# Kernel tuning notes

Hardware: AMD Instinct MI355X
Metric: run time of the kernel (lower is better)

## Reference

```python
import jax, jax.numpy as jnp
import numpy as np

EMBED, VOCAB, NUM_DIGEST, EXPAND = 128, 50257, 4, 4


def _mueller_hash(k):
    # https://stackoverflow.com/a/12996028 , uint32 wraparound semantics
    k = (k >> np.uint32(16) ^ k) * np.uint32(73244475)
    k = (k >> np.uint32(16) ^ k) * np.uint32(73244475)
    k = k >> np.uint32(16) ^ k
    return k


def setup_inputs() -> dict:
    key = jax.random.key(0)
    k_tok, k_tab, k_w1, k_w2 = jax.random.split(key, 4)
    # bloom ledger hash indices (exact replication of bloom_ledger)
    ids = np.arange(VOCAB, dtype=np.uint32)
    i_list, j_list = [], []
    for _ in range(NUM_DIGEST):
        ids = _mueller_hash(ids)
        i_list.append(ids % VOCAB)
        ids = _mueller_hash(ids)
        j_list.append(ids % VOCAB)
    bloom_i = jnp.asarray(np.concatenate(i_list).astype(np.int32))
    bloom_j = jnp.asarray(np.concatenate(j_list).astype(np.int32))
    hidden = EMBED * EXPAND
    return {
        "tokens": jax.random.randint(k_tok, (8, 4096), 0, VOCAB, dtype=jnp.int32),
        "table": jax.random.normal(k_tab, (VOCAB, EMBED), jnp.float32) / np.sqrt(EMBED),
        "bloom_i": bloom_i,
        "bloom_j": bloom_j,
        "w1": jax.random.normal(k_w1, (EMBED, hidden), jnp.float32) / np.sqrt(EMBED),
        "b1": jnp.zeros((hidden,), jnp.float32),
        "w2": jax.random.normal(k_w2, (hidden, EMBED), jnp.float32) / np.sqrt(hidden),
        "b2": jnp.zeros((EMBED,), jnp.float32),
    }


def reference(tokens, table, bloom_i, bloom_j, w1, b1, w2, b2):
    vocab = table.shape[0]
    num_digest = bloom_i.shape[0] // vocab
    scale = jnp.asarray(1.0 / np.sqrt(num_digest), table.dtype)
    # bloom @ table as a scatter-add: A[i] += scale * table[j]  -> [vocab, embed]
    agg = jnp.zeros_like(table).at[bloom_i].add(scale * table[bloom_j])
    # one_hot(tokens) @ (bloom @ table) == row gather
    x = agg[tokens]                      # [B, S, embed]
    h = jax.nn.gelu(x @ w1 + b1)         # [B, S, hidden]
    return h @ w2 + b2                   # [B, S, embed]
```

## Files before the change

### kernel.cpp

```cpp
#include <hip/hip_runtime.h>
#include <hip/hip_bf16.h>
#include <stdint.h>

#define EMBED  128
#define HIDDEN 512
#define TB     64
#define HHALF  256
#define CAP    32

typedef __attribute__((ext_vector_type(8))) short short8v;
typedef __attribute__((ext_vector_type(8))) ushort ushort8v;
typedef __attribute__((ext_vector_type(4))) float f32x4;

__device__ __forceinline__ ushort f2bf(float f) {
    uint32_t b = __float_as_uint(f);
    uint32_t r = (b + 0x7FFFu + ((b >> 16) & 1u)) >> 16;
    return (ushort)r;
}
__device__ __forceinline__ float bf2f(ushort u) {
    return __uint_as_float(((uint32_t)u) << 16);
}

__device__ __forceinline__ float gelu_fast(float x) {
    float x2 = x * x;
    float u  = x * fmaf(0.035677408136f, x2, 0.7978845608f);
    float t  = __expf(2.0f * u);
    return x - x * __frcp_rn(t + 1.0f);
}

__global__ void zero_kernel(int* __restrict__ p, int n) {
    int i = blockIdx.x * blockDim.x + threadIdx.x;
    if (i < n) p[i] = 0;
}

__global__ __launch_bounds__(256)
void prep_kernel(const float* __restrict__ w1, const float* __restrict__ w2,
                 ushort* __restrict__ W1t, ushort* __restrict__ W2t,
                 const float* __restrict__ table, ushort* __restrict__ tbf, int n8, int cb,
                 const int* __restrict__ bi, const int* __restrict__ bj, int nk,
                 int* __restrict__ cnt, ushort* __restrict__ csr) {
    __shared__ float T[32][33];
    int b = blockIdx.x;
    int t = threadIdx.x;
    if (b < 128) {
        const float* in; ushort* outp; int inCols, outCols, tr, tc;
        if (b < 64) {
            in = w1; outp = W1t; inCols = 512; outCols = 128;
            tr = b >> 4; tc = b & 15;
        } else {
            int b2 = b - 64;
            in = w2; outp = W2t; inCols = 128; outCols = 512;
            tr = b2 >> 2; tc = b2 & 3;
        }
        int r  = t >> 3;
        int c4 = (t & 7) * 4;
        float4 v = *(const float4*)&in[(size_t)(tr * 32 + r) * inCols + tc * 32 + c4];
        T[c4 + 0][r] = v.x; T[c4 + 1][r] = v.y; T[c4 + 2][r] = v.z; T[c4 + 3][r] = v.w;
        __syncthreads();
        ushort o[4];
        #pragma unroll
        for (int i = 0; i < 4; ++i) o[i] = f2bf(T[r][c4 + i]);
        *(ushort4*)&outp[(size_t)(tc * 32 + r) * outCols + tr * 32 + c4] = *(ushort4*)o;
    } else if (b < 128 + cb) {
        int gid = (b - 128) * 256 + t;
        if (gid < n8) {
            const float* src = table + (size_t)gid * 8;
            float4 v0 = *(const float4*)(src);
            float4 v1 = *(const float4*)(src + 4);
            ushort u[8] = {f2bf(v0.x), f2bf(v0.y), f2bf(v0.z), f2bf(v0.w),
                           f2bf(v1.x), f2bf(v1.y), f2bf(v1.z), f2bf(v1.w)};
            *(short8v*)&tbf[(size_t)gid * 8] = *(short8v*)u;
        }
    } else {
        int k = (b - 128 - cb) * 256 + t;
        if (k < nk) {
            int i = bi[k];
            int slot = atomicAdd(&cnt[i], 1);
            if (slot < CAP) csr[(size_t)i * CAP + slot] = (ushort)bj[k];
        }
    }
}

__global__ __launch_bounds__(512)
void mlp_mfma_kernel(const int*    __restrict__ tokens,
                     const ushort* __restrict__ tbf,
                     const int*    __restrict__ cnt,
                     const ushort* __restrict__ csr,
                     const ushort* __restrict__ W1t,
                     const ushort* __restrict__ W2t,
                     const float*  __restrict__ b1,
                     const float*  __restrict__ b2,
                     float*        __restrict__ out) {
    __shared__ ushort Xs[TB * EMBED];
    __shared__ ushort Hs[TB * HHALF];

    const int t    = threadIdx.x;
    const int lane = t & 63;
    const int wv   = t >> 6;
    const int base = blockIdx.x * TB;
    const int l15  = lane & 15;
    const int lhi  = lane >> 4;

    {
        int r    = t >> 3;
        int c16  = t & 7;
        int tok  = tokens[base + r];
        int m    = min(cnt[tok], CAP);
        const ushort* jrow = csr + (size_t)tok * CAP;
        ushort8v jv = *(const ushort8v*)jrow;

        short8v v[8][2];
        #pragma unroll
        for (int e = 0; e < 8; ++e) {
            int j = (e < m) ? (int)jv[e] : 0;
            const ushort* trp = tbf + (size_t)j * EMBED + c16 * 16;
            v[e][0] = *(const short8v*)(trp);
            v[e][1] = *(const short8v*)(trp + 8);
        }
        float acc[16] = {0.f,0.f,0.f,0.f,0.f,0.f,0.f,0.f,
                         0.f,0.f,0.f,0.f,0.f,0.f,0.f,0.f};
        #pragma unroll
        for (int e = 0; e < 8; ++e) {
            if (e < m) {
                #pragma unroll
                for (int q = 0; q < 8; ++q) {
                    acc[q]     += bf2f((ushort)v[e][0][q]);
                    acc[8 + q] += bf2f((ushort)v[e][1][q]);
                }
            }
        }
        for (int e = 8; e < m; ++e) {
            int j = (int)jrow[e];
            const ushort* trp = tbf + (size_t)j * EMBED + c16 * 16;
            short8v w0 = *(const short8v*)(trp);
            short8v w1 = *(const short8v*)(trp + 8);
            #pragma unroll
            for (int q = 0; q < 8; ++q) {
                acc[q]     += bf2f((ushort)w0[q]);
                acc[8 + q] += bf2f((ushort)w1[q]);
            }
        }
        ushort u[16];
        #pragma unroll
        for (int q = 0; q < 16; ++q) u[q] = f2bf(0.5f * acc[q]);
        int g0 = c16 * 2;
        #pragma unroll
        for (int h = 0; h < 2; ++h)
            *(short8v*)&Xs[r * EMBED + ((g0 + h) ^ (r & 7)) * 8] = *(short8v*)&u[h * 8];
    }
    __syncthreads();

    f32x4 acc2[4];
    {
        float bv = b2[wv * 16 + l15];
        #pragma unroll
        for (int m = 0; m < 4; ++m) acc2[m] = (f32x4){bv, bv, bv, bv};
    }

    #pragma unroll
    for (int h = 0; h < 2; ++h) {
        f32x4 acc1[4][2];
        #pragma unroll
        for (int n = 0; n < 2; ++n) {
            float bv = b1[h * HHALF + wv * 32 + n * 16 + l15];
            #pragma unroll
            for (int m = 0; m < 4; ++m) acc1[m][n] = (f32x4){bv, bv, bv, bv};
        }
        #pragma unroll
        for (int kk = 0; kk < EMBED / 32; ++kk) {
            short8v a[4];
            #pragma unroll
            for (int m = 0; m < 4; ++m) {
                int r = m * 16 + l15;
                int g = (kk * 4 + lhi) ^ (r & 7);
                a[m] = *(const short8v*)&Xs[r * EMBED + g * 8];
            }
            #pragma unroll
            for (int n = 0; n < 2; ++n) {
                int col = h * HHALF + wv * 32 + n * 16 + l15;
                short8v b = *(const short8v*)(W1t + (size_t)col * EMBED + kk * 32 + lhi * 8);
                #pragma unroll
                for (int m = 0; m < 4; ++m)
                    acc1[m][n] = __builtin_amdgcn_mfma_f32_16x16x32_bf16(a[m], b, acc1[m][n], 0, 0, 0);
            }
        }

        #pragma unroll
        for (int n = 0; n < 2; ++n) {
            int colh = wv * 32 + n * 16 + l15;
            #pragma unroll
            for (int m = 0; m < 4; ++m)
                #pragma unroll
                for (int q = 0; q < 4; ++q) {
                    int row = m * 16 + lhi * 4 + q;
                    float hv = gelu_fast(acc1[m][n][q]);
                    int g = (colh >> 3) ^ (row & 7);
                    Hs[row * HHALF + g * 8 + (colh & 7)] = f2bf(hv);
                }
        }
        __syncthreads();

        #pragma unroll
        for (int kk = 0; kk < HHALF / 32; ++kk) {
            short8v a[4];
            #pragma unroll
            for (int m = 0; m < 4; ++m) {
                int r = m * 16 + l15;
                int g = (kk * 4 + lhi) ^ (r & 7);
                a[m] = *(const short8v*)&Hs[r * HHALF + g * 8];
            }
            int col = wv * 16 + l15;
            short8v b = *(const short8v*)(W2t + (size_t)col * HIDDEN + h * HHALF + kk * 32 + lhi * 8);
            #pragma unroll
            for (int m = 0; m < 4; ++m)
                acc2[m] = __builtin_amdgcn_mfma_f32_16x16x32_bf16(a[m], b, acc2[m], 0, 0, 0);
        }
        __syncthreads();
    }

    #pragma unroll
    for (int m = 0; m < 4; ++m)
        #pragma unroll
        for (int q = 0; q < 4; ++q) {
            int row = m * 16 + lhi * 4 + q;
            out[(size_t)(base + row) * EMBED + wv * 16 + l15] = acc2[m][q];
        }
}

extern "C" void kernel_launch(void* const* d_in, const int* in_sizes, int n_in,
                              void* d_out, int out_size, void* d_ws, size_t ws_size,
                              hipStream_t stream) {
    const int*   tokens = (const int*)  d_in[0];
    const float* table  = (const float*)d_in[1];
    const int*   bi     = (const int*)  d_in[2];
    const int*   bj     = (const int*)  d_in[3];
    const float* w1     = (const float*)d_in[4];
    const float* b1     = (const float*)d_in[5];
    const float* w2     = (const float*)d_in[6];
    const float* b2     = (const float*)d_in[7];
    float* out = (float*)d_out;

    const int vocab = in_sizes[1] / EMBED;
    const int nk    = in_sizes[2];
    const int ntok  = in_sizes[0];

    char* ws = (char*)d_ws;
    size_t off = 0;
    auto alloc = [&](size_t b) { size_t o = off; off += (b + 255) & ~(size_t)255; return o; };
    ushort* W1t = (ushort*)(ws + alloc((size_t)EMBED * HIDDEN * 2));
    ushort* W2t = (ushort*)(ws + alloc((size_t)EMBED * HIDDEN * 2));
    ushort* tbf = (ushort*)(ws + alloc((size_t)vocab * EMBED * 2));
    ushort* csr = (ushort*)(ws + alloc((size_t)vocab * CAP * 2));
    int*    cnt = (int*)   (ws + alloc((size_t)vocab * 4));

    zero_kernel<<<(vocab + 255) / 256, 256, 0, stream>>>(cnt, vocab);

    int n8 = vocab * EMBED / 8;
    int cb = (n8 + 255) / 256;
    int bb = (nk + 255) / 256;
    prep_kernel<<<128 + cb + bb, 256, 0, stream>>>(w1, w2, W1t, W2t,
                                                   table, tbf, n8, cb,
                                                   bi, bj, nk, cnt, csr);

    mlp_mfma_kernel<<<ntok / TB, 512, 0, stream>>>(tokens, tbf, cnt, csr,
                                                   W1t, W2t, b1, b2, out);
}
```

Baseline: 58.47 us.

## Split bloom gather into separate kernel writing bf16 rows before MLP

Moves the per-token bloom aggregation (CSR lookup, gather of table rows, sum, bf16 convert) out of the MLP kernel into a standalone gather kernel, with 16 threads per token each handling 8 columns. The aggregated rows go to a workspace buffer, which the MLP kernel then loads straight into shared memory. The aim is to spread the latency-bound random gathers across many small blocks for better parallelism, instead of stalling the 512-thread MFMA blocks. The cost is an extra kernel launch and a global write and read of the intermediate activations.

```diff
diff --git a/kernel.cpp b/kernel.cpp
--- a/kernel.cpp
+++ b/kernel.cpp
@@ -81,11 +81,48 @@
     }
 }
 
+__global__ void gather_kernel(const int*    __restrict__ tokens,
+                              const ushort* __restrict__ tbf,
+                              const int*    __restrict__ cnt,
+                              const ushort* __restrict__ csr,
+                              ushort*       __restrict__ xrow, int ntok) {
+    int gid = blockIdx.x * blockDim.x + threadIdx.x;
+    int idx = gid >> 4;
+    int c8  = gid & 15;
+    if (idx >= ntok) return;
+    int tok = tokens[idx];
+    int m   = min(cnt[tok], CAP);
+    const ushort* jrow = csr + (size_t)tok * CAP;
+    ushort8v jv = *(const ushort8v*)jrow;
+
+    short8v v[8];
+    #pragma unroll
+    for (int e = 0; e < 8; ++e) {
+        int j = (e < m) ? (int)jv[e] : 0;
+        v[e] = *(const short8v*)&tbf[(size_t)j * EMBED + c8 * 8];
+    }
+    float acc[8] = {0.f,0.f,0.f,0.f,0.f,0.f,0.f,0.f};
+    #pragma unroll
+    for (int e = 0; e < 8; ++e) {
+        if (e < m) {
+            #pragma unroll
+            for (int q = 0; q < 8; ++q) acc[q] += bf2f((ushort)v[e][q]);
+        }
+    }
+    for (int e = 8; e < m; ++e) {
+        int j = (int)jrow[e];
+        short8v w = *(const short8v*)&tbf[(size_t)j * EMBED + c8 * 8];
+        #pragma unroll
+        for (int q = 0; q < 8; ++q) acc[q] += bf2f((ushort)w[q]);
+    }
+    ushort u[8];
+    #pragma unroll
+    for (int q = 0; q < 8; ++q) u[q] = f2bf(0.5f * acc[q]);
+    *(short8v*)&xrow[(size_t)idx * EMBED + c8 * 8] = *(short8v*)u;
+}
+
 __global__ __launch_bounds__(512)
-void mlp_mfma_kernel(const int*    __restrict__ tokens,
-                     const ushort* __restrict__ tbf,
-                     const int*    __restrict__ cnt,
-                     const ushort* __restrict__ csr,
+void mlp_mfma_kernel(const ushort* __restrict__ xrow,
                      const ushort* __restrict__ W1t,
                      const ushort* __restrict__ W2t,
                      const float*  __restrict__ b1,
@@ -102,51 +139,15 @@
     const int lhi  = lane >> 4;
 
     {
-        int r    = t >> 3;
-        int c16  = t & 7;
-        int tok  = tokens[base + r];
-        int m    = min(cnt[tok], CAP);
-        const ushort* jrow = csr + (size_t)tok * CAP;
-        ushort8v jv = *(const ushort8v*)jrow;
-
-        short8v v[8][2];
-        #pragma unroll
-        for (int e = 0; e < 8; ++e) {
-            int j = (e < m) ? (int)jv[e] : 0;
-            const ushort* trp = tbf + (size_t)j * EMBED + c16 * 16;
-            v[e][0] = *(const short8v*)(trp);
-            v[e][1] = *(const short8v*)(trp + 8);
-        }
-        float acc[16] = {0.f,0.f,0.f,0.f,0.f,0.f,0.f,0.f,
-                         0.f,0.f,0.f,0.f,0.f,0.f,0.f,0.f};
-        #pragma unroll
-        for (int e = 0; e < 8; ++e) {
-            if (e < m) {
-                #pragma unroll
-                for (int q = 0; q < 8; ++q) {
-                    acc[q]     += bf2f((ushort)v[e][0][q]);
-                    acc[8 + q] += bf2f((ushort)v[e][1][q]);
-                }
-            }
-        }
-        for (int e = 8; e < m; ++e) {
-            int j = (int)jrow[e];
-            const ushort* trp = tbf + (size_t)j * EMBED + c16 * 16;
-            short8v w0 = *(const short8v*)(trp);
-            short8v w1 = *(const short8v*)(trp + 8);
-            #pragma unroll
-            for (int q = 0; q < 8; ++q) {
-                acc[q]     += bf2f((ushort)w0[q]);
-                acc[8 + q] += bf2f((ushort)w1[q]);
-            }
-        }
-        ushort u[16];
-        #pragma unroll
-        for (int q = 0; q < 16; ++q) u[q] = f2bf(0.5f * acc[q]);
-        int g0 = c16 * 2;
-        #pragma unroll
-        for (int h = 0; h < 2; ++h)
-            *(short8v*)&Xs[r * EMBED + ((g0 + h) ^ (r & 7)) * 8] = *(short8v*)&u[h * 8];
+        int r  = t >> 3;
+        int g0 = (t & 7) * 2;
+        const ushort* src = xrow + (size_t)(base + r) * EMBED;
+        #pragma unroll
+        for (int h = 0; h < 2; ++h) {
+            int g = g0 + h;
+            short8v v = *(const short8v*)(src + g * 8);
+            *(short8v*)&Xs[r * EMBED + (g ^ (r & 7)) * 8] = v;
+        }
     }
     __syncthreads();
 
@@ -247,11 +248,12 @@
     char* ws = (char*)d_ws;
     size_t off = 0;
     auto alloc = [&](size_t b) { size_t o = off; off += (b + 255) & ~(size_t)255; return o; };
-    ushort* W1t = (ushort*)(ws + alloc((size_t)EMBED * HIDDEN * 2));
-    ushort* W2t = (ushort*)(ws + alloc((size_t)EMBED * HIDDEN * 2));
-    ushort* tbf = (ushort*)(ws + alloc((size_t)vocab * EMBED * 2));
-    ushort* csr = (ushort*)(ws + alloc((size_t)vocab * CAP * 2));
-    int*    cnt = (int*)   (ws + alloc((size_t)vocab * 4));
+    ushort* W1t  = (ushort*)(ws + alloc((size_t)EMBED * HIDDEN * 2));
+    ushort* W2t  = (ushort*)(ws + alloc((size_t)EMBED * HIDDEN * 2));
+    ushort* tbf  = (ushort*)(ws + alloc((size_t)vocab * EMBED * 2));
+    ushort* xrow = (ushort*)(ws + alloc((size_t)ntok * EMBED * 2));
+    ushort* csr  = (ushort*)(ws + alloc((size_t)vocab * CAP * 2));
+    int*    cnt  = (int*)   (ws + alloc((size_t)vocab * 4));
 
     zero_kernel<<<(vocab + 255) / 256, 256, 0, stream>>>(cnt, vocab);
 
@@ -262,6 +264,8 @@
                                                    table, tbf, n8, cb,
                                                    bi, bj, nk, cnt, csr);
 
-    mlp_mfma_kernel<<<ntok / TB, 512, 0, stream>>>(tokens, tbf, cnt, csr,
-                                                   W1t, W2t, b1, b2, out);
-}
+    gather_kernel<<<(ntok * 16 + 255) / 256, 256, 0, stream>>>(tokens, tbf, cnt, csr,
+                                                               xrow, ntok);
+
+    mlp_mfma_kernel<<<ntok / TB, 512, 0, stream>>>(xrow, W1t, W2t, b1, b2, out);
+}
```

Result: slower. 62.16 us (+6.3%).
